# Kernel optimization log

Hardware: AMD Instinct MI355X
Metric: run time of the kernel (lower is better)

Reference implementation:

```python
import jax, jax.numpy as jnp
import numpy as np

N = 50000; E = 800000; IN_DIM = 128; HID = 128; OUT = 128; K_TARGET = 5000


def setup_inputs() -> dict:
    key = jax.random.key(0)
    ks = jax.random.split(key, 7)
    x = jax.random.normal(ks[0], (N, IN_DIM), jnp.float32)
    edge_index = jax.random.randint(ks[1], (2, E), 0, N, dtype=jnp.int32)
    W1 = jax.random.normal(ks[2], (IN_DIM, HID), jnp.float32) / np.float32(np.sqrt(IN_DIM))
    b1 = jnp.zeros((HID,), jnp.float32)
    W2 = jax.random.normal(ks[3], (HID, OUT), jnp.float32) / np.float32(np.sqrt(HID))
    b2 = jnp.zeros((OUT,), jnp.float32)
    w_score = jax.random.normal(ks[4], (HID,), jnp.float32) / np.float32(np.sqrt(HID))
    W_skip = jax.random.normal(ks[5], (HID, OUT), jnp.float32) / np.float32(np.sqrt(HID))
    b_skip = jnp.zeros((OUT,), jnp.float32)
    return dict(x=x, edge_index=edge_index, W1=W1, b1=b1, W2=W2, b2=b2,
                w_score=w_score, W_skip=W_skip, b_skip=b_skip)


def _gcn(h_in, row, col, W, b, nseg, edge_w=None):
    # PyG GCNConv with add_self_loops=True, normalize=True:
    # deg[i] = sum of incoming edge weights at col + 1 (self loop, weight 1)
    h = h_in @ W
    w = edge_w if edge_w is not None else jnp.ones(row.shape, h.dtype)
    deg = jax.ops.segment_sum(w, col, num_segments=nseg) + 1.0
    dinv = jax.lax.rsqrt(deg)
    norm = dinv[row] * w * dinv[col]                     # [E]
    agg = jax.ops.segment_sum(norm[:, None] * h[row], col, num_segments=nseg)
    agg = agg + (dinv * dinv)[:, None] * h               # self-loop messages
    return agg + b


def _forward(x, edge_index, W1, b1, W2, b2, w_score, W_skip, b_skip):
    row, col = edge_index[0], edge_index[1]
    n = x.shape[0]
    e = row.shape[0]
    x1 = jax.nn.relu(_gcn(x, row, col, W1, b1, n))       # conv1 + relu (dropout: eval mode)
    raw = x1 @ w_score                                    # [N]
    x1g = x1 * jnp.tanh(raw)[:, None]                     # gated features
    K = min(K_TARGET, n)
    _, kept = jax.lax.top_k(raw, K)                       # sorted desc, ties -> lower index
    keep_mask = jnp.zeros((n,), bool).at[kept].set(True)
    deg = jax.ops.segment_sum(jnp.ones((e,), jnp.int32), row, num_segments=n)  # bincount(row)
    # neighbor insertion order: edge i appends col[i] to neigh[row[i]] (order 2i),
    # then row[i] to neigh[col[i]] (order 2i+1)
    owners = jnp.concatenate([row, col])
    neighs = jnp.concatenate([col, row])
    e_ar = jnp.arange(e, dtype=jnp.int32)
    order = jnp.concatenate([2 * e_ar, 2 * e_ar + 1])
    M = 2 * e + 2
    valid = keep_mask[neighs]
    comp = deg[neighs] * M + (M - 1 - order)
    comp = jnp.where(valid, comp, -1)
    best = jax.ops.segment_max(comp, owners, num_segments=n)
    has_valid = best >= 0
    is_best = valid & (comp == best[owners])              # unique per owner (order unique)
    best_neigh = jax.ops.segment_max(jnp.where(is_best, neighs, -1), owners, num_segments=n)
    cluster_of = jnp.full((n,), -1, jnp.int32).at[kept].set(jnp.arange(K, dtype=jnp.int32))
    best_global_kept = kept[jnp.argmax(deg[kept])]
    fallback = cluster_of[best_global_kept]
    assigned = jnp.where(has_valid, cluster_of[jnp.maximum(best_neigh, 0)], fallback)
    cluster_id = jnp.where(keep_mask, cluster_of, assigned)
    # mean pool per cluster (Kc == K since kept nodes carry ids 0..K-1)
    sums = jax.ops.segment_sum(x1g, cluster_id, num_segments=K)
    counts = jnp.maximum(jax.ops.segment_sum(jnp.ones((n,), x.dtype), cluster_id, num_segments=K), 1.0)
    x_p = sums / counts[:, None]
    # coarse edges: duplicates summed == unique edges weighted by counts; self-pairs dropped
    cu, cv = cluster_id[row], cluster_id[col]
    w_e = (cu != cv).astype(x.dtype)
    x_p = _gcn(x_p, cu, cv, W2, b2, K, edge_w=w_e)        # conv2 with edge_weight
    logits = x_p[cluster_id] + x1 @ W_skip + b_skip       # broadcast up + skip
    return logits


def reference(x, edge_index, W1, b1, W2, b2, w_score, W_skip, b_skip):
    logits = _forward(x, edge_index, W1, b1, W2, b2, w_score, W_skip, b_skip)
    return (logits, 0.0)
```

## Files before the change

### kernel.cpp

```cpp
#include <hip/hip_runtime.h>
#include <cstdint>

#define N_NODES 50000
#define N_EDGES 800000
#define DIM 128
#define KSEL 5000
#define MCONST (2 * N_EDGES + 2)
#define PCH 64
#define CANDCAP 8192
#define TM 4
#define KRB ((KSEL + 255) / 256)

typedef unsigned long long u64;
typedef uint32_t u32;

#define FMA4(A_, S_, W_) { (A_).x = fmaf((S_), (W_).x, (A_).x); (A_).y = fmaf((S_), (W_).y, (A_).y); \
                           (A_).z = fmaf((S_), (W_).z, (A_).z); (A_).w = fmaf((S_), (W_).w, (A_).w); }

__device__ __forceinline__ void gemm_tile_body(const float4* __restrict__ W4,
                                               float xs[32][DIM], float4 acc[TM],
                                               int tx, int ty) {
#pragma unroll 8
  for (int k4 = 0; k4 < 32; k4++) {
    float4 xv[TM];
#pragma unroll
    for (int m = 0; m < TM; m++) xv[m] = *(const float4*)&xs[ty + 8 * m][k4 * 4];
#pragma unroll
    for (int j = 0; j < 4; j++) {
      float4 wv = W4[(k4 * 4 + j) * 32 + tx];
#pragma unroll
      for (int m = 0; m < TM; m++) {
        float sv = (j == 0) ? xv[m].x : (j == 1) ? xv[m].y : (j == 2) ? xv[m].z : xv[m].w;
        FMA4(acc[m], sv, wv);
      }
    }
  }
}

__global__ void gemm_tiled(const float* __restrict__ X, const float* __restrict__ W,
                           float* __restrict__ Y, int nrows) {
  __shared__ float xs[32][DIM];
  int tx = threadIdx.x & 31, ty = threadIdx.x >> 5;
  int rbase = blockIdx.x * 32;
  int nval = min(32, nrows - rbase);
  const float4* X4 = (const float4*)(X + (size_t)rbase * DIM);
  float4* xs4 = (float4*)&xs[0][0];
  for (int i = threadIdx.x; i < 32 * 32; i += 256)
    if ((i >> 5) < nval) xs4[i] = X4[i];
  __syncthreads();
  float4 acc[TM];
#pragma unroll
  for (int m = 0; m < TM; m++) acc[m] = make_float4(0.f, 0.f, 0.f, 0.f);
  gemm_tile_body((const float4*)W, xs, acc, tx, ty);
#pragma unroll
  for (int m = 0; m < TM; m++) {
    int r = rbase + ty + 8 * m;
    if (r < nrows) ((float4*)(Y + (size_t)r * DIM))[tx] = acc[m];
  }
}

__global__ void gemm_tiled_div(const float* __restrict__ S, const int* __restrict__ counts,
                               const float* __restrict__ W, float* __restrict__ Y, int nrows) {
  __shared__ float xs[32][DIM];
  int tx = threadIdx.x & 31, ty = threadIdx.x >> 5;
  int rbase = blockIdx.x * 32;
  int nval = min(32, nrows - rbase);
  const float4* X4 = (const float4*)(S + (size_t)rbase * DIM);
  float4* xs4 = (float4*)&xs[0][0];
  for (int i = threadIdx.x; i < 32 * 32; i += 256) {
    int rr = i >> 5;
    if (rr < nval) {
      float inv = 1.0f / (float)max(counts[rbase + rr], 1);
      float4 v = X4[i];
      v.x *= inv; v.y *= inv; v.z *= inv; v.w *= inv;
      xs4[i] = v;
    }
  }
  __syncthreads();
  float4 acc[TM];
#pragma unroll
  for (int m = 0; m < TM; m++) acc[m] = make_float4(0.f, 0.f, 0.f, 0.f);
  gemm_tile_body((const float4*)W, xs, acc, tx, ty);
#pragma unroll
  for (int m = 0; m < TM; m++) {
    int r = rbase + ty + 8 * m;
    if (r < nrows) ((float4*)(Y + (size_t)r * DIM))[tx] = acc[m];
  }
}

__global__ void final_tiled(const float* __restrict__ x1, const float* __restrict__ Wsk,
                            const float* __restrict__ bsk, const float* __restrict__ xp2,
                            const int* __restrict__ cluster, float* __restrict__ out) {
  __shared__ float xs[32][DIM];
  int tx = threadIdx.x & 31, ty = threadIdx.x >> 5;
  int rbase = blockIdx.x * 32;
  int nval = min(32, N_NODES - rbase);
  const float4* X4 = (const float4*)(x1 + (size_t)rbase * DIM);
  float4* xs4 = (float4*)&xs[0][0];
  for (int i = threadIdx.x; i < 32 * 32; i += 256)
    if ((i >> 5) < nval) xs4[i] = X4[i];
  __syncthreads();
  float4 acc[TM];
#pragma unroll
  for (int m = 0; m < TM; m++) acc[m] = make_float4(0.f, 0.f, 0.f, 0.f);
  gemm_tile_body((const float4*)Wsk, xs, acc, tx, ty);
  float4 bv = ((const float4*)bsk)[tx];
#pragma unroll
  for (int m = 0; m < TM; m++) {
    int r = rbase + ty + 8 * m;
    if (r < N_NODES) {
      int cl = cluster[r];
      cl = (cl < 0) ? 0 : (cl >= KSEL ? KSEL - 1 : cl);
      float4 pv = ((const float4*)(xp2 + (size_t)cl * DIM))[tx];
      float4 o;
      o.x = acc[m].x + bv.x + pv.x;
      o.y = acc[m].y + bv.y + pv.y;
      o.z = acc[m].z + bv.z + pv.z;
      o.w = acc[m].w + bv.w + pv.w;
      ((float4*)(out + (size_t)r * DIM))[tx] = o;
    }
  }
  if (blockIdx.x == 0 && threadIdx.x == 0) out[(size_t)N_NODES * DIM] = 0.0f;
}

__global__ void deg_kernel(const int* __restrict__ row, const int* __restrict__ col,
                           int* deg1, int* deg2) {
  int e = blockIdx.x * blockDim.x + threadIdx.x;
  if (e < N_EDGES) {
    atomicAdd(&deg1[col[e]], 1);
    atomicAdd(&deg2[row[e]], 1);
  }
}

__global__ void rsqrt_kernel(const int* __restrict__ deg, float* __restrict__ dinv, int n) {
  int i = blockIdx.x * blockDim.x + threadIdx.x;
  if (i < n) dinv[i] = rsqrtf((float)deg[i] + 1.0f);
}

__global__ void scan_local(const int* __restrict__ in, int* __restrict__ out,
                           int* __restrict__ bsum, int n) {
  __shared__ int s[256];
  int i = blockIdx.x * 256 + threadIdx.x;
  int v = (i < n) ? in[i] : 0;
  s[threadIdx.x] = v;
  __syncthreads();
  for (int off = 1; off < 256; off <<= 1) {
    int t = (threadIdx.x >= off) ? s[threadIdx.x - off] : 0;
    __syncthreads();
    s[threadIdx.x] += t;
    __syncthreads();
  }
  if (i < n) out[i] = s[threadIdx.x] - v;
  if (threadIdx.x == 255) bsum[blockIdx.x] = s[255];
}

__global__ void scan_bsum(int* bsum, int nb) {
  __shared__ int s[256];
  int v = (threadIdx.x < nb) ? bsum[threadIdx.x] : 0;
  s[threadIdx.x] = v;
  __syncthreads();
  for (int off = 1; off < 256; off <<= 1) {
    int t = (threadIdx.x >= off) ? s[threadIdx.x - off] : 0;
    __syncthreads();
    s[threadIdx.x] += t;
    __syncthreads();
  }
  if (threadIdx.x < nb) bsum[threadIdx.x] = s[threadIdx.x] - v;
}

__global__ void scan_add(int* out, const int* __restrict__ bsum, int n) {
  int i = blockIdx.x * 256 + threadIdx.x;
  if (i < n) out[i] += bsum[blockIdx.x];
}

__global__ void scan_small(const int* __restrict__ in, int* __restrict__ out, int n) {
  __shared__ int s[256];
  __shared__ int carry;
  if (threadIdx.x == 0) carry = 0;
  __syncthreads();
  for (int base = 0; base < n; base += 256) {
    int i = base + threadIdx.x;
    int v = (i < n) ? in[i] : 0;
    s[threadIdx.x] = v;
    __syncthreads();
    for (int off = 1; off < 256; off <<= 1) {
      int t = (threadIdx.x >= off) ? s[threadIdx.x - off] : 0;
      __syncthreads();
      s[threadIdx.x] += t;
      __syncthreads();
    }
    int c = carry;
    if (i < n) out[i] = c + s[threadIdx.x] - v;
    __syncthreads();
    if (threadIdx.x == 255) carry = c + s[255];
    __syncthreads();
  }
  if (threadIdx.x == 0) out[n] = carry;
}

__global__ void fill_ecsr(const int* __restrict__ row, const int* __restrict__ col,
                          const int* __restrict__ start, int* cursor, int* payload) {
  int e = blockIdx.x * blockDim.x + threadIdx.x;
  if (e < N_EDGES) {
    int c = col[e];
    int p = start[c] + atomicAdd(&cursor[c], 1);
    if (p >= 0 && p < N_EDGES) payload[p] = row[e];
  }
}

__global__ void fill_members(const int* __restrict__ cluster, const int* __restrict__ startn,
                             int* cursorn, int* members) {
  int i = blockIdx.x * blockDim.x + threadIdx.x;
  if (i < N_NODES) {
    int c = cluster[i];
    int p = startn[c] + atomicAdd(&cursorn[c], 1);
    if (p >= 0 && p < N_NODES) members[p] = i;
  }
}

__global__ void gcn1_gather(const int* __restrict__ srcs, const int* __restrict__ start,
                            const int* __restrict__ deg1, const float* __restrict__ dinv,
                            const float* __restrict__ h, const float* __restrict__ b1,
                            const float* __restrict__ wscore,
                            float* __restrict__ B, float* __restrict__ gate,
                            u64* __restrict__ key) {
  int i = blockIdx.x, t = threadIdx.x;
  int g = t >> 5, lane = t & 31;
  int s0 = start[i], n = deg1[i];
  const float4* h4 = (const float4*)h;
  float4 acc0 = make_float4(0.f, 0.f, 0.f, 0.f);
  float4 acc1 = make_float4(0.f, 0.f, 0.f, 0.f);
  int k = g;
  int ra0 = (k < n) ? srcs[s0 + k] : -1;
  int ra1 = (k + 4 < n) ? srcs[s0 + k + 4] : -1;
  while (ra0 >= 0) {
    int rb0 = (k + 8 < n) ? srcs[s0 + k + 8] : -1;
    int rb1 = (k + 12 < n) ? srcs[s0 + k + 12] : -1;
    float w0 = dinv[ra0];
    float4 hv0 = h4[(size_t)ra0 * 32 + lane];
    if (ra1 >= 0) {
      float w1 = dinv[ra1];
      float4 hv1 = h4[(size_t)ra1 * 32 + lane];
      FMA4(acc0, w0, hv0);
      FMA4(acc1, w1, hv1);
    } else {
      FMA4(acc0, w0, hv0);
    }
    ra0 = rb0; ra1 = rb1; k += 8;
  }
  acc0.x += acc1.x; acc0.y += acc1.y; acc0.z += acc1.z; acc0.w += acc1.w;

  __shared__ float red4[4][DIM];
  *(float4*)&red4[g][lane * 4] = acc0;
  __syncthreads();

  float di = dinv[i];
  float asum = red4[0][t] + red4[1][t] + red4[2][t] + red4[3][t];
  float v = asum * di + di * di * h[(size_t)i * DIM + t] + b1[t];
  v = v > 0.f ? v : 0.f;
  B[(size_t)i * DIM + t] = v;

  __shared__ float red[DIM];
  red[t] = v * wscore[t];
  __syncthreads();
  for (int s = DIM / 2; s > 0; s >>= 1) {
    if (t < s) red[t] += red[t + s];
    __syncthreads();
  }
  if (t == 0) {
    float r = red[0];
    gate[i] = tanhf(r);
    u32 b = __float_as_uint(r);
    if ((b << 1) == 0u) b = 0u;
    u32 ord = (b & 0x80000000u) ? ~b : (b | 0x80000000u);
    key[i] = (((u64)(~ord)) << 32) | (u32)i;
  }
}

__global__ void hist1_kernel(const u64* __restrict__ key, int* __restrict__ hist) {
  int i = blockIdx.x * blockDim.x + threadIdx.x;
  if (i < N_NODES) atomicAdd(&hist[(int)(key[i] >> 52)], 1);
}

__global__ void hist2_kernel(const u64* __restrict__ key, const int* __restrict__ selb,
                             int* __restrict__ hist) {
  int i = blockIdx.x * blockDim.x + threadIdx.x;
  if (i < N_NODES) {
    u64 k = key[i];
    if ((int)(k >> 52) == selb[0]) atomicAdd(&hist[(int)((k >> 40) & 0xFFF)], 1);
  }
}

__global__ void pick_kernel(const int* __restrict__ hist, int K_imm, int* __restrict__ selb,
                            int rem_in_slot, int bin_out_slot, int rem_out_slot) {
  __shared__ int s[256];
  int t = threadIdx.x;
  int base = t * 16;
  int loc[16];
  int sum = 0;
#pragma unroll
  for (int k = 0; k < 16; k++) { loc[k] = hist[base + k]; sum += loc[k]; }
  s[t] = sum;
  __syncthreads();
  for (int off = 1; off < 256; off <<= 1) {
    int v = (t >= off) ? s[t - off] : 0;
    __syncthreads();
    s[t] += v;
    __syncthreads();
  }
  int target = (K_imm >= 0) ? K_imm : selb[rem_in_slot];
  int prev = (t == 0) ? 0 : s[t - 1];
  if (prev < target && target <= s[t]) {
    int cum = prev;
#pragma unroll
    for (int k = 0; k < 16; k++) {
      cum += loc[k];
      if (cum >= target) {
        selb[bin_out_slot] = base + k;
        selb[rem_out_slot] = target - (cum - loc[k]);
        break;
      }
    }
  }
}

__global__ void collect_kernel(const u64* __restrict__ key, const int* __restrict__ selb,
                               u64* __restrict__ cand, int* __restrict__ ccnt) {
  int i = blockIdx.x * blockDim.x + threadIdx.x;
  if (i < N_NODES) {
    u64 k = key[i];
    if ((int)(k >> 52) == selb[0] && (int)((k >> 40) & 0xFFF) == selb[2]) {
      int p = atomicAdd(ccnt, 1);
      if (p < CANDCAP) cand[p] = k;
    }
  }
}

__global__ void thresh_kernel(const u64* __restrict__ cand, const int* __restrict__ ccnt,
                              const int* __restrict__ selb, u64* __restrict__ T) {
  int c = min(*ccnt, CANDCAP);
  int R = selb[3];
  for (int p = threadIdx.x; p < c; p += 256) {
    u64 kp = cand[p];
    int cnt = 0;
    for (int q = 0; q < c; q++) cnt += (cand[q] < kp) ? 1 : 0;
    if (cnt == R - 1) *T = kp;
  }
}

__global__ void compact_kernel(const u64* __restrict__ key, const u64* __restrict__ T,
                               int* __restrict__ krank, u64* __restrict__ kkey,
                               int* __restrict__ kidx, int* __restrict__ kcnt) {
  int i = blockIdx.x * blockDim.x + threadIdx.x;
  if (i < N_NODES) {
    krank[i] = -1;
    u64 k = key[i];
    if (k <= *T) {
      int p = atomicAdd(kcnt, 1);
      if (p < KSEL + 16) {
        kkey[p] = k;
        kidx[p] = i;
      }
    }
  }
}

__global__ void krank_count(const u64* __restrict__ kkey, int* __restrict__ rankc) {
  int p = blockIdx.x * 256 + threadIdx.x;
  u64 mykey = (p < KSEL) ? kkey[p] : ~0ull;
  int qbase = blockIdx.y * 256;
  __shared__ u64 sk[256];
  int j = qbase + threadIdx.x;
  sk[threadIdx.x] = (j < KSEL) ? kkey[j] : ~0ull;
  __syncthreads();
  int lim = min(256, KSEL - qbase);
  int cnt = 0;
#pragma unroll 8
  for (int q = 0; q < lim; q++) cnt += (sk[q] < mykey) ? 1 : 0;
  if (p < KSEL && cnt) atomicAdd(&rankc[p], cnt);
}

__global__ void krank_final(const int* __restrict__ rankc, const int* __restrict__ kidx,
                            const int* __restrict__ deg2, int* __restrict__ krank,
                            u64* fbkey) {
  int p = blockIdx.x * 256 + threadIdx.x;
  if (p < KSEL) {
    int node = kidx[p];
    if (node >= 0 && node < N_NODES) {
      int cnt = rankc[p];
      krank[node] = cnt;
      u64 fk = (((u64)(deg2[node] + 1)) << 32) | (u32)(KSEL - 1 - cnt);
      atomicMax(fbkey, fk);
    }
  }
}

__global__ void bestneigh_kernel(const int* __restrict__ row, const int* __restrict__ col,
                                 const int* __restrict__ krank, const int* __restrict__ deg2,
                                 u64* __restrict__ best) {
  int e = blockIdx.x * blockDim.x + threadIdx.x;
  if (e < N_EDGES) {
    int r = row[e], c = col[e];
    if (krank[c] >= 0) {
      u64 comp = (u64)deg2[c] * (u64)MCONST + (u64)(MCONST - 1 - 2 * e);
      atomicMax(&best[r], comp + 1);
    }
    if (krank[r] >= 0) {
      u64 comp = (u64)deg2[r] * (u64)MCONST + (u64)(MCONST - 2 - 2 * e);
      atomicMax(&best[c], comp + 1);
    }
  }
}

__global__ void assign_kernel(const int* __restrict__ krank, const u64* __restrict__ best,
                              const int* __restrict__ row, const int* __restrict__ col,
                              const u64* __restrict__ fbkey,
                              int* __restrict__ cluster, int* __restrict__ counts) {
  int i = blockIdx.x * blockDim.x + threadIdx.x;
  if (i >= N_NODES) return;
  int c;
  int rk = krank[i];
  if (rk >= 0) {
    c = rk;
  } else {
    u64 b = best[i];
    if (b > 0) {
      u64 comp = b - 1;
      int rem = (int)(comp % (u64)MCONST);
      int ord = MCONST - 1 - rem;
      int e = ord >> 1;
      int nb = (ord & 1) ? row[e] : col[e];
      c = krank[nb];
    } else {
      c = KSEL - 1 - (int)((*fbkey) & 0xffffffffu);
    }
  }
  c = (c < 0) ? 0 : (c >= KSEL ? KSEL - 1 : c);
  cluster[i] = c;
  atomicAdd(&counts[c], 1);
}

__global__ void pool_chunk(const int* __restrict__ members, const int* __restrict__ startn,
                           const float* __restrict__ x1, const float* __restrict__ gate,
                           float* __restrict__ sums) {
  int cb = blockIdx.x * PCH;
  if (cb >= N_NODES) return;
  int ce = min(cb + PCH, N_NODES);
  __shared__ int pl[PCH];
  for (int k = threadIdx.x; k < ce - cb; k += DIM) pl[k] = members[cb + k];
  __syncthreads();
  int lo = 0, hi = KSEL - 1;
  while (lo < hi) { int mid = (lo + hi + 1) >> 1; if (startn[mid] <= cb) lo = mid; else hi = mid - 1; }
  int c = lo;
  int segend = startn[c + 1];
  int t = threadIdx.x;
  float acc = 0.f;
  for (int k = cb; k < ce; k++) {
    int j = pl[k - cb];
    acc = fmaf(gate[j], x1[j * DIM + t], acc);
    int k1 = k + 1;
    if (k1 == segend || k1 == ce) {
      atomicAdd(&sums[c * DIM + t], acc);
      acc = 0.f;
      if (k1 == segend && k1 < ce) {
        while (c < KSEL - 1 && startn[c + 1] <= k1) c++;
        segend = startn[c + 1];
      }
    }
  }
}

__global__ void map_csrc(const int* __restrict__ payload, const int* __restrict__ cluster,
                         int* __restrict__ csrc) {
  int p = blockIdx.x * blockDim.x + threadIdx.x;
  if (p < N_EDGES) csrc[p] = cluster[payload[p]];
}

__global__ void cdeg_kernel(const int* __restrict__ csrc, const int* __restrict__ start,
                            const int* __restrict__ deg1, const int* __restrict__ cluster,
                            int* __restrict__ degc) {
  int v = blockIdx.x * blockDim.x + threadIdx.x;
  if (v >= N_NODES) return;
  int cv = cluster[v];
  int s0 = start[v], n = deg1[v], cnt = 0;
  for (int k = 0; k < n; k++) cnt += (csrc[s0 + k] != cv) ? 1 : 0;
  if (cnt) atomicAdd(&degc[cv], cnt);
}

__global__ void coarse_gather2(const int* __restrict__ csrc, const int* __restrict__ start,
                               const int* __restrict__ deg1, const int* __restrict__ cluster,
                               const float* __restrict__ dinvc, const float* __restrict__ h2,
                               float* __restrict__ agg2) {
  int v = blockIdx.x, t = threadIdx.x;
  int n = deg1[v];
  if (n == 0) return;
  int g = t >> 5, lane = t & 31;
  int cv = cluster[v];
  int s0 = start[v];
  const float4* h24 = (const float4*)h2;
  float4 acc0 = make_float4(0.f, 0.f, 0.f, 0.f);
  float4 acc1 = make_float4(0.f, 0.f, 0.f, 0.f);
  int inter = 0;
  int k = g;
  int ca0 = (k < n) ? csrc[s0 + k] : -1;
  int ca1 = (k + 4 < n) ? csrc[s0 + k + 4] : -1;
  while (ca0 >= 0) {
    int cb0 = (k + 8 < n) ? csrc[s0 + k + 8] : -1;
    int cb1 = (k + 12 < n) ? csrc[s0 + k + 12] : -1;
    float w0 = (ca0 == cv) ? 0.f : dinvc[ca0];
    inter += (ca0 != cv) ? 1 : 0;
    float4 hv0 = h24[(size_t)ca0 * 32 + lane];
    if (ca1 >= 0) {
      float w1 = (ca1 == cv) ? 0.f : dinvc[ca1];
      inter += (ca1 != cv) ? 1 : 0;
      float4 hv1 = h24[(size_t)ca1 * 32 + lane];
      FMA4(acc0, w0, hv0);
      FMA4(acc1, w1, hv1);
    } else {
      FMA4(acc0, w0, hv0);
    }
    ca0 = cb0; ca1 = cb1; k += 8;
  }
  acc0.x += acc1.x; acc0.y += acc1.y; acc0.z += acc1.z; acc0.w += acc1.w;

  __shared__ float red4[4][DIM];
  __shared__ int sinter[4];
  *(float4*)&red4[g][lane * 4] = acc0;
  if (lane == 0) sinter[g] = inter;
  __syncthreads();
  if (sinter[0] + sinter[1] + sinter[2] + sinter[3] == 0) return;
  float sv = red4[0][t] + red4[1][t] + red4[2][t] + red4[3][t];
  atomicAdd(&agg2[(size_t)cv * DIM + t], sv);
}

__global__ void combine2(const float* __restrict__ agg2, const float* __restrict__ h2,
                         const float* __restrict__ dinvc, const float* __restrict__ b2,
                         float* __restrict__ xp2) {
  int gid = blockIdx.x * blockDim.x + threadIdx.x;
  int c = gid >> 7, d = gid & 127;
  if (c < KSEL) {
    float dc = dinvc[c];
    xp2[gid] = agg2[gid] * dc + dc * dc * h2[gid] + b2[d];
  }
}

extern "C" void kernel_launch(void* const* d_in, const int* in_sizes, int n_in,
                              void* d_out, int out_size, void* d_ws, size_t ws_size,
                              hipStream_t stream) {
  const float* x      = (const float*)d_in[0];
  const int*   eidx   = (const int*)d_in[1];
  const float* W1     = (const float*)d_in[2];
  const float* b1     = (const float*)d_in[3];
  const float* W2     = (const float*)d_in[4];
  const float* b2     = (const float*)d_in[5];
  const float* wscore = (const float*)d_in[6];
  const float* Wsk    = (const float*)d_in[7];
  const float* bsk    = (const float*)d_in[8];
  float* out = (float*)d_out;

  const int* row = eidx;
  const int* col = eidx + N_EDGES;

  char* ws = (char*)d_ws;
#define ALIGN16(v) (((v) + 15) & ~(size_t)15)
  size_t off = 0;
#define CARVE(ptr_t, name, bytes) ptr_t name = (ptr_t)(ws + off); off = ALIGN16(off + (bytes))
  size_t h_off = off;
  CARVE(float*, h, (size_t)N_NODES * DIM * 4);
  CARVE(float*, B, (size_t)N_NODES * DIM * 4);
  CARVE(int*, payload, (size_t)N_EDGES * 4);
  CARVE(u64*, key, (size_t)N_NODES * 8);
  CARVE(float*, gate, (size_t)N_NODES * 4);
  CARVE(float*, dinv, (size_t)N_NODES * 4);
  CARVE(int*, start, (size_t)N_NODES * 4);
  CARVE(int*, bsum, 256 * 4);
  size_t zA = off;
  CARVE(int*, deg1, (size_t)N_NODES * 4);
  CARVE(int*, deg2, (size_t)N_NODES * 4);
  CARVE(int*, cursor, (size_t)N_NODES * 4);
  size_t zAsize = off - zA;

  size_t ho = h_off;
#define CARVE2(ptr_t, name, bytes) ptr_t name = (ptr_t)(ws + ho); ho = ALIGN16(ho + (bytes))
  CARVE2(int*, cluster, (size_t)N_NODES * 4);
  CARVE2(int*, members, (size_t)N_NODES * 4);
  CARVE2(int*, startn, (size_t)(KSEL + 1) * 4);
  CARVE2(float*, dinvc, (size_t)KSEL * 4);
  CARVE2(float*, h2, (size_t)KSEL * DIM * 4);
  CARVE2(int*, csrc, (size_t)N_EDGES * 4);
  size_t zB = ho;
  CARVE2(u64*, best, (size_t)N_NODES * 8);
  CARVE2(int*, counts, (size_t)KSEL * 4);
  CARVE2(int*, degc, (size_t)KSEL * 4);
  CARVE2(int*, cursorn, (size_t)KSEL * 4);
  CARVE2(float*, sums, (size_t)KSEL * DIM * 4);
  CARVE2(float*, agg2, (size_t)KSEL * DIM * 4);
  CARVE2(u64*, fbkey, 8);
  CARVE2(int*, hist1, 4096 * 4);
  CARVE2(int*, hist2, 4096 * 4);
  CARVE2(int*, rankc, (size_t)KSEL * 4);
  CARVE2(int*, ccnt, 16);
  CARVE2(int*, kcnt, 16);
  size_t zBsize = ho - zB;
  CARVE2(int*, krank, (size_t)N_NODES * 4);
  CARVE2(u64*, cand, (size_t)CANDCAP * 8);
  CARVE2(u64*, kkey, (size_t)(KSEL + 16) * 8);
  CARVE2(int*, kidx, (size_t)(KSEL + 16) * 4);
  CARVE2(int*, selb, 4 * 4);
  CARVE2(u64*, Tkey, 8);
  float* xp2 = sums;
  (void)ws_size; (void)out_size; (void)n_in; (void)in_sizes;

  const int eb  = (N_EDGES + 255) / 256;
  const int nb  = (N_NODES + 255) / 256;
  const int kbs = (KSEL + 255) / 256;
  const int pcb = (N_NODES + PCH - 1) / PCH;
  const int gtb = (N_NODES + 31) / 32;
  const int gkb = (KSEL + 31) / 32;

  hipMemsetAsync(ws + zA, 0, zAsize, stream);

  gemm_tiled<<<gtb, 256, 0, stream>>>(x, W1, h, N_NODES);
  deg_kernel<<<eb, 256, 0, stream>>>(row, col, deg1, deg2);
  rsqrt_kernel<<<nb, 256, 0, stream>>>(deg1, dinv, N_NODES);
  scan_local<<<nb, 256, 0, stream>>>(deg1, start, bsum, N_NODES);
  scan_bsum<<<1, 256, 0, stream>>>(bsum, nb);
  scan_add<<<nb, 256, 0, stream>>>(start, bsum, N_NODES);
  fill_ecsr<<<eb, 256, 0, stream>>>(row, col, start, cursor, payload);
  gcn1_gather<<<N_NODES, DIM, 0, stream>>>(payload, start, deg1, dinv, h, b1, wscore,
                                           B, gate, key);
  hipMemsetAsync(ws + zB, 0, zBsize, stream);

  hist1_kernel<<<nb, 256, 0, stream>>>(key, hist1);
  pick_kernel<<<1, 256, 0, stream>>>(hist1, KSEL, selb, 0, 0, 1);
  hist2_kernel<<<nb, 256, 0, stream>>>(key, selb, hist2);
  pick_kernel<<<1, 256, 0, stream>>>(hist2, -1, selb, 1, 2, 3);
  collect_kernel<<<nb, 256, 0, stream>>>(key, selb, cand, ccnt);
  thresh_kernel<<<1, 256, 0, stream>>>(cand, ccnt, selb, Tkey);
  compact_kernel<<<nb, 256, 0, stream>>>(key, Tkey, krank, kkey, kidx, kcnt);
  krank_count<<<dim3(KRB, KRB), 256, 0, stream>>>(kkey, rankc);
  krank_final<<<kbs, 256, 0, stream>>>(rankc, kidx, deg2, krank, fbkey);

  bestneigh_kernel<<<eb, 256, 0, stream>>>(row, col, krank, deg2, best);
  assign_kernel<<<nb, 256, 0, stream>>>(krank, best, row, col, fbkey, cluster, counts);

  scan_small<<<1, 256, 0, stream>>>(counts, startn, KSEL);
  fill_members<<<nb, 256, 0, stream>>>(cluster, startn, cursorn, members);
  pool_chunk<<<pcb, DIM, 0, stream>>>(members, startn, B, gate, sums);
  map_csrc<<<eb, 256, 0, stream>>>(payload, cluster, csrc);
  cdeg_kernel<<<nb, 256, 0, stream>>>(csrc, start, deg1, cluster, degc);
  rsqrt_kernel<<<kbs, 256, 0, stream>>>(degc, dinvc, KSEL);

  gemm_tiled_div<<<gkb, 256, 0, stream>>>(sums, counts, W2, h2, KSEL);
  coarse_gather2<<<N_NODES, DIM, 0, stream>>>(csrc, start, deg1, cluster, dinvc, h2, agg2);
  combine2<<<(KSEL * DIM) / 256, 256, 0, stream>>>(agg2, h2, dinvc, b2, xp2);

  final_tiled<<<gtb, 256, 0, stream>>>(B, Wsk, bsk, xp2, cluster, out);
}
```

Measured before the change: 719.0 us.

## Process one node per wavefront with grid-stride loops in GCN gathers

The two gather kernels drop the one-block-per-node launch (50000 blocks of 128 threads) and switch to persistent 64-lane wavefronts over a fixed grid, each looping over nodes with a grid stride. Each wavefront splits neighbours across two half-waves and combines them with cross-lane shuffles, removing shared-memory reductions and __syncthreads. Per-node metadata for the next node is prefetched. The aim is to cut block launch and barrier overhead, at the cost of less memory-level parallelism per node (2 neighbour streams instead of 4) and possible load imbalance on high-degree nodes.

```diff
diff --git a/kernel.cpp b/kernel.cpp
--- a/kernel.cpp
+++ b/kernel.cpp
@@ -10,6 +10,7 @@
 #define CANDCAP 8192
 #define TM 4
 #define KRB ((KSEL + 255) / 256)
+#define GPERS 2048
 
 typedef unsigned long long u64;
 typedef uint32_t u32;
@@ -224,56 +225,71 @@
                             const float* __restrict__ wscore,
                             float* __restrict__ B, float* __restrict__ gate,
                             u64* __restrict__ key) {
-  int i = blockIdx.x, t = threadIdx.x;
-  int g = t >> 5, lane = t & 31;
-  int s0 = start[i], n = deg1[i];
+  int lane = threadIdx.x & 63;
+  int g = lane >> 5, l32 = lane & 31;
+  int wid = blockIdx.x * (blockDim.x >> 6) + (threadIdx.x >> 6);
+  int nw = gridDim.x * (blockDim.x >> 6);
   const float4* h4 = (const float4*)h;
-  float4 acc0 = make_float4(0.f, 0.f, 0.f, 0.f);
-  float4 acc1 = make_float4(0.f, 0.f, 0.f, 0.f);
-  int k = g;
-  int ra0 = (k < n) ? srcs[s0 + k] : -1;
-  int ra1 = (k + 4 < n) ? srcs[s0 + k + 4] : -1;
-  while (ra0 >= 0) {
-    int rb0 = (k + 8 < n) ? srcs[s0 + k + 8] : -1;
-    int rb1 = (k + 12 < n) ? srcs[s0 + k + 12] : -1;
-    float w0 = dinv[ra0];
-    float4 hv0 = h4[(size_t)ra0 * 32 + lane];
-    if (ra1 >= 0) {
-      float w1 = dinv[ra1];
-      float4 hv1 = h4[(size_t)ra1 * 32 + lane];
-      FMA4(acc0, w0, hv0);
-      FMA4(acc1, w1, hv1);
-    } else {
-      FMA4(acc0, w0, hv0);
-    }
-    ra0 = rb0; ra1 = rb1; k += 8;
-  }
-  acc0.x += acc1.x; acc0.y += acc1.y; acc0.z += acc1.z; acc0.w += acc1.w;
-
-  __shared__ float red4[4][DIM];
-  *(float4*)&red4[g][lane * 4] = acc0;
-  __syncthreads();
-
-  float di = dinv[i];
-  float asum = red4[0][t] + red4[1][t] + red4[2][t] + red4[3][t];
-  float v = asum * di + di * di * h[(size_t)i * DIM + t] + b1[t];
-  v = v > 0.f ? v : 0.f;
-  B[(size_t)i * DIM + t] = v;
-
-  __shared__ float red[DIM];
-  red[t] = v * wscore[t];
-  __syncthreads();
-  for (int s = DIM / 2; s > 0; s >>= 1) {
-    if (t < s) red[t] += red[t + s];
-    __syncthreads();
-  }
-  if (t == 0) {
-    float r = red[0];
-    gate[i] = tanhf(r);
-    u32 b = __float_as_uint(r);
-    if ((b << 1) == 0u) b = 0u;
-    u32 ord = (b & 0x80000000u) ? ~b : (b | 0x80000000u);
-    key[i] = (((u64)(~ord)) << 32) | (u32)i;
+  float4 wsv = ((const float4*)wscore)[l32];
+  float4 b1v = ((const float4*)b1)[l32];
+  int v = wid;
+  int s0 = 0, n = 0; float di = 0.f;
+  if (v < N_NODES) { s0 = start[v]; n = deg1[v]; di = dinv[v]; }
+  while (v < N_NODES) {
+    int vn = v + nw;
+    int s0n = 0, nn = 0; float din = 0.f;
+    if (vn < N_NODES) { s0n = start[vn]; nn = deg1[vn]; din = dinv[vn]; }
+    float4 hself = h4[(size_t)v * 32 + l32];
+    float4 acc0 = make_float4(0.f, 0.f, 0.f, 0.f);
+    float4 acc1 = make_float4(0.f, 0.f, 0.f, 0.f);
+    int k = g;
+    int ra0 = (k < n) ? srcs[s0 + k] : -1;
+    int ra1 = (k + 2 < n) ? srcs[s0 + k + 2] : -1;
+    while (ra0 >= 0) {
+      int rb0 = (k + 4 < n) ? srcs[s0 + k + 4] : -1;
+      int rb1 = (k + 6 < n) ? srcs[s0 + k + 6] : -1;
+      float w0 = dinv[ra0];
+      float4 hv0 = h4[(size_t)ra0 * 32 + l32];
+      if (ra1 >= 0) {
+        float w1 = dinv[ra1];
+        float4 hv1 = h4[(size_t)ra1 * 32 + l32];
+        FMA4(acc0, w0, hv0);
+        FMA4(acc1, w1, hv1);
+      } else {
+        FMA4(acc0, w0, hv0);
+      }
+      ra0 = rb0; ra1 = rb1; k += 4;
+    }
+    acc0.x += acc1.x; acc0.y += acc1.y; acc0.z += acc1.z; acc0.w += acc1.w;
+    acc0.x += __shfl_xor(acc0.x, 32);
+    acc0.y += __shfl_xor(acc0.y, 32);
+    acc0.z += __shfl_xor(acc0.z, 32);
+    acc0.w += __shfl_xor(acc0.w, 32);
+    float dd = di * di;
+    float4 vv;
+    vv.x = acc0.x * di + dd * hself.x + b1v.x;
+    vv.y = acc0.y * di + dd * hself.y + b1v.y;
+    vv.z = acc0.z * di + dd * hself.z + b1v.z;
+    vv.w = acc0.w * di + dd * hself.w + b1v.w;
+    vv.x = vv.x > 0.f ? vv.x : 0.f;
+    vv.y = vv.y > 0.f ? vv.y : 0.f;
+    vv.z = vv.z > 0.f ? vv.z : 0.f;
+    vv.w = vv.w > 0.f ? vv.w : 0.f;
+    if (lane < 32) ((float4*)(B + (size_t)v * DIM))[l32] = vv;
+    float sd = vv.x * wsv.x + vv.y * wsv.y + vv.z * wsv.z + vv.w * wsv.w;
+    sd += __shfl_xor(sd, 1);
+    sd += __shfl_xor(sd, 2);
+    sd += __shfl_xor(sd, 4);
+    sd += __shfl_xor(sd, 8);
+    sd += __shfl_xor(sd, 16);
+    if (lane == 0) {
+      gate[v] = tanhf(sd);
+      u32 b = __float_as_uint(sd);
+      if ((b << 1) == 0u) b = 0u;
+      u32 ord = (b & 0x80000000u) ? ~b : (b | 0x80000000u);
+      key[v] = (((u64)(~ord)) << 32) | (u32)v;
+    }
+    v = vn; s0 = s0n; n = nn; di = din;
   }
 }
 
@@ -491,46 +507,56 @@
                                const int* __restrict__ deg1, const int* __restrict__ cluster,
                                const float* __restrict__ dinvc, const float* __restrict__ h2,
                                float* __restrict__ agg2) {
-  int v = blockIdx.x, t = threadIdx.x;
-  int n = deg1[v];
-  if (n == 0) return;
-  int g = t >> 5, lane = t & 31;
-  int cv = cluster[v];
-  int s0 = start[v];
+  int lane = threadIdx.x & 63;
+  int g = lane >> 5, l32 = lane & 31;
+  int wid = blockIdx.x * (blockDim.x >> 6) + (threadIdx.x >> 6);
+  int nw = gridDim.x * (blockDim.x >> 6);
   const float4* h24 = (const float4*)h2;
-  float4 acc0 = make_float4(0.f, 0.f, 0.f, 0.f);
-  float4 acc1 = make_float4(0.f, 0.f, 0.f, 0.f);
-  int inter = 0;
-  int k = g;
-  int ca0 = (k < n) ? csrc[s0 + k] : -1;
-  int ca1 = (k + 4 < n) ? csrc[s0 + k + 4] : -1;
-  while (ca0 >= 0) {
-    int cb0 = (k + 8 < n) ? csrc[s0 + k + 8] : -1;
-    int cb1 = (k + 12 < n) ? csrc[s0 + k + 12] : -1;
-    float w0 = (ca0 == cv) ? 0.f : dinvc[ca0];
-    inter += (ca0 != cv) ? 1 : 0;
-    float4 hv0 = h24[(size_t)ca0 * 32 + lane];
-    if (ca1 >= 0) {
-      float w1 = (ca1 == cv) ? 0.f : dinvc[ca1];
-      inter += (ca1 != cv) ? 1 : 0;
-      float4 hv1 = h24[(size_t)ca1 * 32 + lane];
-      FMA4(acc0, w0, hv0);
-      FMA4(acc1, w1, hv1);
-    } else {
-      FMA4(acc0, w0, hv0);
-    }
-    ca0 = cb0; ca1 = cb1; k += 8;
-  }
-  acc0.x += acc1.x; acc0.y += acc1.y; acc0.z += acc1.z; acc0.w += acc1.w;
-
-  __shared__ float red4[4][DIM];
-  __shared__ int sinter[4];
-  *(float4*)&red4[g][lane * 4] = acc0;
-  if (lane == 0) sinter[g] = inter;
-  __syncthreads();
-  if (sinter[0] + sinter[1] + sinter[2] + sinter[3] == 0) return;
-  float sv = red4[0][t] + red4[1][t] + red4[2][t] + red4[3][t];
-  atomicAdd(&agg2[(size_t)cv * DIM + t], sv);
+  int v = wid;
+  int s0 = 0, n = 0, cv = 0;
+  if (v < N_NODES) { s0 = start[v]; n = deg1[v]; cv = cluster[v]; }
+  while (v < N_NODES) {
+    int vn = v + nw;
+    int s0n = 0, nn = 0, cvn = 0;
+    if (vn < N_NODES) { s0n = start[vn]; nn = deg1[vn]; cvn = cluster[vn]; }
+    float4 acc0 = make_float4(0.f, 0.f, 0.f, 0.f);
+    float4 acc1 = make_float4(0.f, 0.f, 0.f, 0.f);
+    int inter = 0;
+    int k = g;
+    int ca0 = (k < n) ? csrc[s0 + k] : -1;
+    int ca1 = (k + 2 < n) ? csrc[s0 + k + 2] : -1;
+    while (ca0 >= 0) {
+      int cb0 = (k + 4 < n) ? csrc[s0 + k + 4] : -1;
+      int cb1 = (k + 6 < n) ? csrc[s0 + k + 6] : -1;
+      float w0 = (ca0 == cv) ? 0.f : dinvc[ca0];
+      inter += (ca0 != cv) ? 1 : 0;
+      float4 hv0 = h24[(size_t)ca0 * 32 + l32];
+      if (ca1 >= 0) {
+        float w1 = (ca1 == cv) ? 0.f : dinvc[ca1];
+        inter += (ca1 != cv) ? 1 : 0;
+        float4 hv1 = h24[(size_t)ca1 * 32 + l32];
+        FMA4(acc0, w0, hv0);
+        FMA4(acc1, w1, hv1);
+      } else {
+        FMA4(acc0, w0, hv0);
+      }
+      ca0 = cb0; ca1 = cb1; k += 4;
+    }
+    acc0.x += acc1.x; acc0.y += acc1.y; acc0.z += acc1.z; acc0.w += acc1.w;
+    acc0.x += __shfl_xor(acc0.x, 32);
+    acc0.y += __shfl_xor(acc0.y, 32);
+    acc0.z += __shfl_xor(acc0.z, 32);
+    acc0.w += __shfl_xor(acc0.w, 32);
+    int itot = inter + __shfl_xor(inter, 32);
+    if (itot > 0 && lane < 32) {
+      float* dst = agg2 + (size_t)cv * DIM + l32 * 4;
+      atomicAdd(dst + 0, acc0.x);
+      atomicAdd(dst + 1, acc0.y);
+      atomicAdd(dst + 2, acc0.z);
+      atomicAdd(dst + 3, acc0.w);
+    }
+    v = vn; s0 = s0n; n = nn; cv = cvn;
+  }
 }
 
 __global__ void combine2(const float* __restrict__ agg2, const float* __restrict__ h2,
@@ -627,8 +653,8 @@
   scan_bsum<<<1, 256, 0, stream>>>(bsum, nb);
   scan_add<<<nb, 256, 0, stream>>>(start, bsum, N_NODES);
   fill_ecsr<<<eb, 256, 0, stream>>>(row, col, start, cursor, payload);
-  gcn1_gather<<<N_NODES, DIM, 0, stream>>>(payload, start, deg1, dinv, h, b1, wscore,
-                                           B, gate, key);
+  gcn1_gather<<<GPERS, 256, 0, stream>>>(payload, start, deg1, dinv, h, b1, wscore,
+                                         B, gate, key);
   hipMemsetAsync(ws + zB, 0, zBsize, stream);
 
   hist1_kernel<<<nb, 256, 0, stream>>>(key, hist1);
@@ -652,7 +678,7 @@
   rsqrt_kernel<<<kbs, 256, 0, stream>>>(degc, dinvc, KSEL);
 
   gemm_tiled_div<<<gkb, 256, 0, stream>>>(sums, counts, W2, h2, KSEL);
-  coarse_gather2<<<N_NODES, DIM, 0, stream>>>(csrc, start, deg1, cluster, dinvc, h2, agg2);
+  coarse_gather2<<<GPERS, 256, 0, stream>>>(csrc, start, deg1, cluster, dinvc, h2, agg2);
   combine2<<<(KSEL * DIM) / 256, 256, 0, stream>>>(agg2, h2, dinvc, b2, xp2);
 
   final_tiled<<<gtb, 256, 0, stream>>>(B, Wsk, bsk, xp2, cluster, out);
```

Measured after the change: 930.5 us. +29.4%, slower.
